# Performance work log

Hardware: AMD Instinct MI355X
Metric: run time of the kernel (lower is better)

## Reference

```python
import jax, jax.numpy as jnp
import numpy as np

D_MODEL = 1024
NUM_HEADS = 16
NUM_GROUPS = 4
HEAD_DIM = D_MODEL // NUM_HEADS
ROPE_BASE = 10000.0


def _rope_tables(seq_len, head_dim, dtype=jnp.float32):
    inv_freq = 1.0 / (ROPE_BASE ** (jnp.arange(0, head_dim, 2, dtype=jnp.float32) / head_dim))
    freqs = jnp.arange(seq_len, dtype=jnp.float32)[:, None] * inv_freq[None, :]  # [S, hd/2]
    emb = jnp.concatenate([freqs, freqs], axis=-1)  # [S, hd]
    return jnp.cos(emb).astype(dtype), jnp.sin(emb).astype(dtype)


def _rotate_half(t):
    half = t.shape[-1] // 2
    return jnp.concatenate([-t[..., half:], t[..., :half]], axis=-1)


def _apply_rope(t, cos, sin):
    # t: [B,S,H,hd]; cos/sin: [S,hd] broadcast over batch and heads
    c = cos[None, :, None, :]
    s = sin[None, :, None, :]
    return t * c + _rotate_half(t) * s


def setup_inputs() -> dict:
    key = jax.random.key(0)
    ks = jax.random.split(key, 5)
    B, S, D = 2, 2048, D_MODEL
    scale = 1.0 / np.sqrt(D)
    return {
        "x": jax.random.normal(ks[0], (B, S, D), dtype=jnp.float32),
        "Wq": jax.random.normal(ks[1], (D, D), dtype=jnp.float32) * scale,
        "Wk": jax.random.normal(ks[2], (D, D), dtype=jnp.float32) * scale,
        "Wv": jax.random.normal(ks[3], (D, D), dtype=jnp.float32) * scale,
        "Wo": jax.random.normal(ks[4], (D, D), dtype=jnp.float32) * scale,
    }


def reference(x, Wq, Wk, Wv, Wo):
    B, S, D = x.shape
    H, G, hd = NUM_HEADS, NUM_GROUPS, HEAD_DIM
    hpg = H // G  # heads per group

    q = (x @ Wq.T).reshape(B, S, H, hd)
    k = (x @ Wk.T).reshape(B, S, H, hd)
    v = (x @ Wv.T).reshape(B, S, H, hd)

    cos, sin = _rope_tables(S, hd, x.dtype)
    q = _apply_rope(q, cos, sin)
    k = _apply_rope(k, cos, sin)

    # query head reordering: [B,S,G,hpg,hd] -> transpose(2,3) -> [B,S,H,hd]
    q = q.reshape(B, S, G, hpg, hd).swapaxes(2, 3).reshape(B, S, H, hd)
    # GQA group-mean of K/V, then repeat back to H heads
    k = k.reshape(B, S, G, hpg, hd).mean(axis=3)  # [B,S,G,hd]
    v = v.reshape(B, S, G, hpg, hd).mean(axis=3)
    k = jnp.repeat(k, hpg, axis=2)  # [B,S,H,hd]
    v = jnp.repeat(v, hpg, axis=2)

    q = q.transpose(0, 2, 1, 3)  # [B,H,S,hd]
    k = k.transpose(0, 2, 1, 3)
    v = v.transpose(0, 2, 1, 3)

    scores = jnp.einsum('bhqd,bhkd->bhqk', q, k) / np.sqrt(hd)  # [B,H,S,S]
    probs = jax.nn.softmax(scores, axis=-1)
    attn = jnp.einsum('bhqk,bhkd->bhqd', probs, v)

    attn = attn.transpose(0, 2, 1, 3).reshape(B, S, D)
    return attn @ Wo.T
```

## Files before the change

kernel.cpp:

```cpp
#include <hip/hip_runtime.h>
#include <hip/hip_bf16.h>
#include <math.h>

#define B_ 2
#define S_ 2048
#define D_ 1024
#define H_ 16
#define G_ 4
#define HD_ 64

typedef float f32x4  __attribute__((ext_vector_type(4)));
typedef float f32x16 __attribute__((ext_vector_type(16)));
typedef short s16x8  __attribute__((ext_vector_type(8)));
typedef unsigned short u16x4 __attribute__((ext_vector_type(4)));
typedef unsigned int   u32x4 __attribute__((ext_vector_type(4)));

__device__ __forceinline__ unsigned short f2b(float f) {
    __hip_bfloat16 h = __float2bfloat16(f);
    return __builtin_bit_cast(unsigned short, h);
}
__device__ __forceinline__ unsigned cvtpk(float lo, float hi) {
    unsigned r;
    asm("v_cvt_pk_bf16_f32 %0, %1, %2" : "=v"(r) : "v"(lo), "v"(hi));
    return r;
}
__device__ __forceinline__ void plswap(unsigned &a, unsigned &b) {
    asm("v_permlane32_swap_b32 %0, %1" : "+v"(a), "+v"(b));
}

#define MFMA16(a, b, c) __builtin_amdgcn_mfma_f32_16x16x32_bf16(a, b, c, 0, 0, 0)
#define MFMA32(a, b, c) __builtin_amdgcn_mfma_f32_32x32x16_bf16(a, b, c, 0, 0, 0)

#define GLOAD16(gp, lp) __builtin_amdgcn_global_load_lds(                      \
    (const __attribute__((address_space(1))) void*)(gp),                      \
    (__attribute__((address_space(3))) void*)(lp), 16, 0, 0)

__global__ __launch_bounds__(256)
void prep_all(const float* __restrict__ x,  const float* __restrict__ Wq,
              const float* __restrict__ Wk, const float* __restrict__ Wv,
              const float* __restrict__ Wo,
              unsigned short* __restrict__ xb, unsigned short* __restrict__ wb,
              unsigned short* __restrict__ wob,
              float* __restrict__ cost, float* __restrict__ sint)
{
    const int NQ_WB = (1536*1024)/4;
    const int NQ_WO = (1024*1024)/4;
    const int NQ_X  = (B_*S_*D_)/4;
    int q = blockIdx.x*256 + threadIdx.x;
    if (q < NQ_WB) {
        const int idx = q*4, row = idx >> 10, c = idx & 1023;
        u16x4 o;
        if (row < 1024) {
            f32x4 v = *(const f32x4*)&Wq[(size_t)row*1024 + c];
            #pragma unroll
            for (int j = 0; j < 4; ++j) o[j] = f2b(v[j]);
        } else {
            const int rd = row - 1024, kv = rd >> 8, gd = rd & 255;
            const int g = gd >> 6, d = gd & 63;
            const float* W = kv ? Wv : Wk;
            f32x4 sum = {0.f, 0.f, 0.f, 0.f};
            #pragma unroll
            for (int p = 0; p < 4; ++p)
                sum += *(const f32x4*)&W[(size_t)((g*4 + p)*64 + d)*1024 + c];
            #pragma unroll
            for (int j = 0; j < 4; ++j) o[j] = f2b(sum[j]*0.25f);
        }
        *(u16x4*)&wb[idx] = o;
        return;
    }
    q -= NQ_WB;
    if (q < NQ_WO) {
        const int idx = q*4;
        f32x4 v = *(const f32x4*)&Wo[idx];
        u16x4 o;
        #pragma unroll
        for (int j = 0; j < 4; ++j) o[j] = f2b(v[j]);
        *(u16x4*)&wob[idx] = o;
        return;
    }
    q -= NQ_WO;
    if (q < NQ_X) {
        const int idx = q*4;
        f32x4 v = *(const f32x4*)&x[idx];
        u16x4 o;
        #pragma unroll
        for (int j = 0; j < 4; ++j) o[j] = f2b(v[j]);
        *(u16x4*)&xb[idx] = o;
        return;
    }
    q -= NQ_X;
    if (q < (S_*32)/4) {
        const int idx = q*4, s = idx >> 5, f0 = idx & 31;
        #pragma unroll
        for (int j = 0; j < 4; ++j) {
            const float f = (float)(f0 + j);
            const float fr = (float)s * powf(10000.0f, -f*(1.0f/32.0f));
            cost[idx + j] = cosf(fr);
            sint[idx + j] = sinf(fr);
        }
    }
}

template<int MODE>
__global__ __launch_bounds__(256)
void gemm_mfma(const unsigned short* __restrict__ Am,
               const unsigned short* __restrict__ Bm,
               unsigned short* __restrict__ qr,
               unsigned short* __restrict__ kr,
               unsigned short* __restrict__ vt,
               float* __restrict__ outf,
               const float* __restrict__ cost,
               const float* __restrict__ sint,
               int nbx)
{
    __shared__ unsigned short As[2][128*64];
    __shared__ unsigned short Bs[2][128*64];

    const int nwg = gridDim.x;
    const int cpx = nwg >> 3;
    const int bid = blockIdx.x;
    const int swz = (bid & 7)*cpx + (bid >> 3);
    const int bx = swz % nbx, by = swz / nbx;

    const int t  = threadIdx.x;
    const int w  = t >> 6, l = t & 63;
    const int lg = l >> 4, lr = l & 15;
    const int wr = w >> 1, wc = w & 1;

    const unsigned short* gA = Am + (size_t)by*128*D_;
    const unsigned short* gB = Bm + (size_t)bx*128*D_;

    const int srow = l >> 3;
    const int schk = (l & 7) ^ srow;

#define STAGE(buf, k0)                                                         \
    _Pragma("unroll")                                                          \
    for (int i_ = 0; i_ < 4; ++i_) {                                           \
        const int row_ = 32*w + 8*i_ + srow;                                   \
        GLOAD16(gA + (size_t)row_*D_ + (k0) + 8*schk, &As[buf][(32*w + 8*i_)*64]); \
        GLOAD16(gB + (size_t)row_*D_ + (k0) + 8*schk, &Bs[buf][(32*w + 8*i_)*64]); \
    }

    f32x4 acc[4][4] = {};

    STAGE(0, 0);
    #pragma unroll 1
    for (int kt = 0; kt < 16; ++kt) {
        const int cur = kt & 1;
        if (kt < 15) {
            STAGE(cur ^ 1, 64*(kt + 1));
            asm volatile("s_waitcnt vmcnt(8)" ::: "memory");
        } else {
            asm volatile("s_waitcnt vmcnt(0)" ::: "memory");
        }
        __builtin_amdgcn_s_barrier();

        #pragma unroll
        for (int kk = 0; kk < 2; ++kk) {
            s16x8 af[4], bfr[4];
            #pragma unroll
            for (int m = 0; m < 4; ++m) {
                const int row = 64*wr + 16*m + lr;
                af[m] = *(const s16x8*)&As[cur][row*64 + 8*((lg + 4*kk) ^ (row & 7))];
            }
            #pragma unroll
            for (int n = 0; n < 4; ++n) {
                const int col = 64*wc + 16*n + lr;
                bfr[n] = *(const s16x8*)&Bs[cur][col*64 + 8*((lg + 4*kk) ^ (col & 7))];
            }
            #pragma unroll
            for (int m = 0; m < 4; ++m)
                #pragma unroll
                for (int n = 0; n < 4; ++n)
                    acc[m][n] = MFMA16(af[m], bfr[n], acc[m][n]);
        }
        asm volatile("s_waitcnt lgkmcnt(0)" ::: "memory");
        __builtin_amdgcn_s_barrier();
    }
#undef STAGE

    if (MODE == 1) {
        #pragma unroll
        for (int m = 0; m < 4; ++m)
            #pragma unroll
            for (int r = 0; r < 4; ++r) {
                const int row = by*128 + 64*wr + 16*m + 4*lg + r;
                #pragma unroll
                for (int n = 0; n < 4; ++n)
                    outf[(size_t)row*D_ + bx*128 + 64*wc + 16*n + lr] = acc[m][n][r];
            }
        return;
    }

    if (bx < 10) {
        const float CQ = 0.18033688011112044f;
        #pragma unroll
        for (int m = 0; m < 4; ++m) {
            #pragma unroll
            for (int r = 0; r < 4; ++r) {
                const int row = by*128 + 64*wr + 16*m + 4*lg + r;
                const int b = row >> 11, s = row & (S_ - 1);
                const float c_lo = cost[s*32 + lr],      s_lo = sint[s*32 + lr];
                const float c_hi = cost[s*32 + 16 + lr], s_hi = sint[s*32 + 16 + lr];
                unsigned short vals[4];
                #pragma unroll
                for (int n = 0; n < 4; ++n) {
                    const float cc = (n & 1) ? c_hi : c_lo;
                    const float sn = (n & 1) ? s_hi : s_lo;
                    const float self = acc[m][n][r], part = acc[m][n ^ 2][r];
                    float rv = (n < 2) ? fmaf(self, cc, -part*sn)
                                       : fmaf(self, cc,  part*sn);
                    if (bx < 8) rv *= CQ;
                    vals[n] = f2b(rv);
                }
                size_t base;
                unsigned short* dst;
                if (bx < 8) {
                    const int hh = 2*bx + wc;
                    const int hp = (hh & 3)*4 + (hh >> 2);
                    base = (((size_t)b*H_ + hp)*S_ + s)*HD_;
                    dst = qr;
                } else {
                    const int g = (bx - 8)*2 + wc;
                    base = (((size_t)b*G_ + g)*S_ + s)*HD_;
                    dst = kr;
                }
                #pragma unroll
                for (int n = 0; n < 4; ++n) dst[base + 16*n + lr] = vals[n];
            }
        }
    } else {
        const int g = (bx - 10)*2 + wc;
        #pragma unroll
        for (int m = 0; m < 4; ++m) {
            const int row0 = by*128 + 64*wr + 16*m + 4*lg;
            const int b = row0 >> 11, s0 = row0 & (S_ - 1);
            #pragma unroll
            for (int n = 0; n < 4; ++n) {
                const int dd = 16*n + lr;
                u16x4 v;
                #pragma unroll
                for (int r = 0; r < 4; ++r) v[r] = f2b(acc[m][n][r]);
                *(u16x4*)&vt[(((size_t)b*G_ + g)*HD_ + dd)*S_ + s0] = v;
            }
        }
    }
}

__device__ __forceinline__ void stage128(const unsigned short* Kp, const unsigned short* Vp,
                                         unsigned short* ks, unsigned short* vs,
                                         int kt, int w, int l)
{
    const int srow = l >> 3;
    const int schk = (l & 7) ^ srow;
    const int vrow = l >> 4;
    #pragma unroll
    for (int i = 0; i < 4; ++i) {
        const int krow = 32*w + 8*i + srow;
        GLOAD16(Kp + ((size_t)(kt*128 + krow))*HD_ + 8*schk, ks + (32*w + 8*i)*64);
        const int d    = 16*w + 4*i + vrow;
        const int vchk = (l & 15) ^ (d & 7);
        GLOAD16(Vp + (size_t)d*S_ + kt*128 + 8*vchk, vs + (16*w + 4*i)*128);
    }
}

__global__ __launch_bounds__(256)
void flash_attn_mfma(const unsigned short* __restrict__ qr,
                     const unsigned short* __restrict__ kr,
                     const unsigned short* __restrict__ vt,
                     unsigned short* __restrict__ attnb)
{
    __shared__ unsigned short Ks[2][128*64];
    __shared__ unsigned short Vs[2][64*128];

    const int nqt = S_/128;
    const int bid = blockIdx.x;
    const int cpx = gridDim.x >> 3;
    const int swz = (bid & 7)*cpx + (bid >> 3);
    const int qt = swz % nqt;
    const int h  = (swz/nqt) % H_;
    const int b  = swz/(nqt*H_);
    const int g  = h >> 2;
    const int t  = threadIdx.x;
    const int w  = t >> 6;
    const int l  = t & 63;
    const int hi = l >> 5;
    const int li = l & 31;

    const unsigned short* Qp = qr + (((size_t)b*H_ + h)*S_ + (size_t)qt*128 + w*32)*HD_;
    const unsigned short* Kp = kr + ((size_t)b*G_ + g)*(size_t)S_*HD_;
    const unsigned short* Vp = vt + ((size_t)b*G_ + g)*(size_t)HD_*S_;

    s16x8 qf[4];
    #pragma unroll
    for (int kk = 0; kk < 4; ++kk)
        qf[kk] = *(const s16x8*)(Qp + (size_t)li*HD_ + 16*kk + 8*hi);

    s16x8 ones;
    #pragma unroll
    for (int e = 0; e < 8; ++e) ones[e] = (short)0x3F80;

    f32x16 o[2], o_l;
    #pragma unroll
    for (int e = 0; e < 16; ++e) { o[0][e] = 0.f; o[1][e] = 0.f; o_l[e] = 0.f; }

    const int NT = S_/128;
    stage128(Kp, Vp, Ks[0], Vs[0], 0, w, l);

    #pragma unroll 1
    for (int kt = 0; kt < NT; ++kt) {
        const int cur = kt & 1;
        if (kt + 1 < NT) {
            stage128(Kp, Vp, Ks[cur^1], Vs[cur^1], kt + 1, w, l);
            asm volatile("s_waitcnt vmcnt(8)" ::: "memory");
        } else {
            asm volatile("s_waitcnt vmcnt(0)" ::: "memory");
        }
        __builtin_amdgcn_s_barrier();

        f32x16 sc[4];
        #pragma unroll
        for (int q4 = 0; q4 < 4; ++q4)
            #pragma unroll
            for (int e = 0; e < 16; ++e) sc[q4][e] = 0.f;

        __builtin_amdgcn_s_setprio(1);
        #pragma unroll
        for (int kk = 0; kk < 4; ++kk) {
            const int chk = 8*((hi + 2*kk) ^ (li & 7));
            #pragma unroll
            for (int q4 = 0; q4 < 4; ++q4) {
                s16x8 kf = *(const s16x8*)&Ks[cur][(32*q4 + li)*64 + chk];
                sc[q4] = MFMA32(kf, qf[kk], sc[q4]);
            }
        }
        __builtin_amdgcn_s_setprio(0);

        #pragma unroll
        for (int q4 = 0; q4 < 4; ++q4)
            #pragma unroll
            for (int e = 0; e < 16; ++e)
                sc[q4][e] = __builtin_amdgcn_exp2f(sc[q4][e]);

        __builtin_amdgcn_s_setprio(1);
        #pragma unroll
        for (int q4 = 0; q4 < 4; ++q4) {
            #pragma unroll
            for (int s2 = 0; s2 < 2; ++s2) {
                unsigned a0 = cvtpk(sc[q4][8*s2+0], sc[q4][8*s2+1]);
                unsigned a1 = cvtpk(sc[q4][8*s2+2], sc[q4][8*s2+3]);
                unsigned a2 = cvtpk(sc[q4][8*s2+4], sc[q4][8*s2+5]);
                unsigned a3 = cvtpk(sc[q4][8*s2+6], sc[q4][8*s2+7]);
                plswap(a0, a2); plswap(a1, a3);
                u32x4 aw = {a0, a1, a2, a3};
                s16x8 paf = __builtin_bit_cast(s16x8, aw);
                const int ks = 2*q4 + s2;
                #pragma unroll
                for (int dt = 0; dt < 2; ++dt) {
                    const int d = li + 32*dt;
                    s16x8 vf = *(const s16x8*)&Vs[cur][d*128 + 8*((hi + 2*ks) ^ (li & 7))];
                    o[dt] = MFMA32(paf, vf, o[dt]);
                }
                o_l = MFMA32(paf, ones, o_l);
            }
        }
        __builtin_amdgcn_s_setprio(0);

        asm volatile("s_waitcnt lgkmcnt(0)" ::: "memory");
        __builtin_amdgcn_s_barrier();
    }

    #pragma unroll
    for (int r = 0; r < 16; ++r) {
        const int qq = (r & 3) + 8*(r >> 2) + 4*hi;
        const int s  = qt*128 + w*32 + qq;
        const float inv = 1.0f / o_l[r];
        #pragma unroll
        for (int dt = 0; dt < 2; ++dt)
            attnb[((size_t)b*S_ + s)*D_ + h*HD_ + li + 32*dt] = f2b(o[dt][r]*inv);
    }
}

extern "C" void kernel_launch(void* const* d_in, const int* in_sizes, int n_in,
                              void* d_out, int out_size, void* d_ws, size_t ws_size,
                              hipStream_t stream)
{
    const float* x  = (const float*)d_in[0];
    const float* Wq = (const float*)d_in[1];
    const float* Wk = (const float*)d_in[2];
    const float* Wv = (const float*)d_in[3];
    const float* Wo = (const float*)d_in[4];
    float* out = (float*)d_out;

    char* p = (char*)d_ws;
    unsigned short* xb    = (unsigned short*)p; p += (size_t)B_*S_*D_*2;
    unsigned short* wb    = (unsigned short*)p; p += (size_t)1536*1024*2;
    unsigned short* wob   = (unsigned short*)p; p += (size_t)1024*1024*2;
    unsigned short* qr    = (unsigned short*)p; p += (size_t)B_*H_*S_*HD_*2;
    unsigned short* kr    = (unsigned short*)p; p += (size_t)B_*G_*S_*HD_*2;
    unsigned short* vt    = (unsigned short*)p; p += (size_t)B_*G_*HD_*S_*2;
    unsigned short* attnb = (unsigned short*)p; p += (size_t)B_*S_*D_*2;
    float* cost = (float*)p; p += (size_t)S_*32*4;
    float* sint = (float*)p;

    prep_all<<<6720, 256, 0, stream>>>(x, Wq, Wk, Wv, Wo, xb, wb, wob, cost, sint);
    gemm_mfma<0><<<32*12, 256, 0, stream>>>(xb, wb, qr, kr, vt, nullptr, cost, sint, 12);
    flash_attn_mfma<<<B_*H_*(S_/128), 256, 0, stream>>>(qr, kr, vt, attnb);
    gemm_mfma<1><<<32*8, 256, 0, stream>>>(attnb, wob, nullptr, nullptr, nullptr, out, cost, sint, 8);
}
```

Measured before the change: 100.5 us.

## Split attention over key halves with a combine kernel and smaller key tiles

Each attention block now processes half of the key sequence with 64-key tiles, doubling the grid, and writes unnormalized partial outputs and row sums. A new combine kernel adds the two halves and normalizes them into the attention buffer. Workspace is rearranged so the partials reuse the region of the consumed bf16 input and weights. This aims at better CU occupancy and latency hiding, at the cost of an extra launch, extra memory traffic and bf16 rounding of the partials.

```diff
diff --git a/kernel.cpp b/kernel.cpp
--- a/kernel.cpp
+++ b/kernel.cpp
@@ -18,6 +18,9 @@
 __device__ __forceinline__ unsigned short f2b(float f) {
     __hip_bfloat16 h = __float2bfloat16(f);
     return __builtin_bit_cast(unsigned short, h);
+}
+__device__ __forceinline__ float b2f(unsigned short u) {
+    return __builtin_bit_cast(float, (unsigned)u << 16);
 }
 __device__ __forceinline__ unsigned cvtpk(float lo, float hi) {
     unsigned r;
@@ -247,49 +250,47 @@
     }
 }
 
-__device__ __forceinline__ void stage128(const unsigned short* Kp, const unsigned short* Vp,
-                                         unsigned short* ks, unsigned short* vs,
-                                         int kt, int w, int l)
+__device__ __forceinline__ void stage64(const unsigned short* Kp, const unsigned short* Vp,
+                                        unsigned short* ks, unsigned short* vs,
+                                        int key0, int w, int l)
 {
     const int srow = l >> 3;
     const int schk = (l & 7) ^ srow;
-    const int vrow = l >> 4;
-    #pragma unroll
-    for (int i = 0; i < 4; ++i) {
-        const int krow = 32*w + 8*i + srow;
-        GLOAD16(Kp + ((size_t)(kt*128 + krow))*HD_ + 8*schk, ks + (32*w + 8*i)*64);
-        const int d    = 16*w + 4*i + vrow;
-        const int vchk = (l & 15) ^ (d & 7);
-        GLOAD16(Vp + (size_t)d*S_ + kt*128 + 8*vchk, vs + (16*w + 4*i)*128);
-    }
-}
-
-__global__ __launch_bounds__(256)
+    #pragma unroll
+    for (int i = 0; i < 2; ++i) {
+        const int row = 16*w + 8*i + srow;
+        GLOAD16(Kp + ((size_t)(key0 + row))*HD_ + 8*schk, ks + (16*w + 8*i)*64);
+        GLOAD16(Vp + (size_t)row*S_ + key0 + 8*schk,      vs + (16*w + 8*i)*64);
+    }
+}
+
+__global__ __launch_bounds__(256, 4)
 void flash_attn_mfma(const unsigned short* __restrict__ qr,
                      const unsigned short* __restrict__ kr,
                      const unsigned short* __restrict__ vt,
-                     unsigned short* __restrict__ attnb)
-{
-    __shared__ unsigned short Ks[2][128*64];
-    __shared__ unsigned short Vs[2][64*128];
-
-    const int nqt = S_/128;
-    const int bid = blockIdx.x;
-    const int cpx = gridDim.x >> 3;
-    const int swz = (bid & 7)*cpx + (bid >> 3);
-    const int qt = swz % nqt;
-    const int h  = (swz/nqt) % H_;
-    const int b  = swz/(nqt*H_);
-    const int g  = h >> 2;
-    const int t  = threadIdx.x;
-    const int w  = t >> 6;
-    const int l  = t & 63;
-    const int hi = l >> 5;
-    const int li = l & 31;
+                     unsigned short* __restrict__ po,
+                     float* __restrict__ pl)
+{
+    __shared__ unsigned short Ks[2][64*64];
+    __shared__ unsigned short Vs[2][64*64];
+
+    const int bid  = blockIdx.x;
+    const int cpx  = gridDim.x >> 3;
+    const int swz  = (bid & 7)*cpx + (bid >> 3);
+    const int qt   = swz & 15;
+    const int h    = (swz >> 4) & 15;
+    const int b    = (swz >> 8) & 1;
+    const int half = swz >> 9;
+    const int g    = h >> 2;
+    const int t    = threadIdx.x;
+    const int w    = t >> 6;
+    const int l    = t & 63;
+    const int hi   = l >> 5;
+    const int li   = l & 31;
 
     const unsigned short* Qp = qr + (((size_t)b*H_ + h)*S_ + (size_t)qt*128 + w*32)*HD_;
-    const unsigned short* Kp = kr + ((size_t)b*G_ + g)*(size_t)S_*HD_;
-    const unsigned short* Vp = vt + ((size_t)b*G_ + g)*(size_t)HD_*S_;
+    const unsigned short* Kp = kr + ((size_t)b*G_ + g)*(size_t)S_*HD_ + (size_t)half*1024*HD_;
+    const unsigned short* Vp = vt + ((size_t)b*G_ + g)*(size_t)HD_*S_ + half*1024;
 
     s16x8 qf[4];
     #pragma unroll
@@ -304,23 +305,23 @@
     #pragma unroll
     for (int e = 0; e < 16; ++e) { o[0][e] = 0.f; o[1][e] = 0.f; o_l[e] = 0.f; }
 
-    const int NT = S_/128;
-    stage128(Kp, Vp, Ks[0], Vs[0], 0, w, l);
+    const int NT = 1024/64;
+    stage64(Kp, Vp, Ks[0], Vs[0], 0, w, l);
 
     #pragma unroll 1
     for (int kt = 0; kt < NT; ++kt) {
         const int cur = kt & 1;
         if (kt + 1 < NT) {
-            stage128(Kp, Vp, Ks[cur^1], Vs[cur^1], kt + 1, w, l);
-            asm volatile("s_waitcnt vmcnt(8)" ::: "memory");
+            stage64(Kp, Vp, Ks[cur^1], Vs[cur^1], 64*(kt + 1), w, l);
+            asm volatile("s_waitcnt vmcnt(4)" ::: "memory");
         } else {
             asm volatile("s_waitcnt vmcnt(0)" ::: "memory");
         }
         __builtin_amdgcn_s_barrier();
 
-        f32x16 sc[4];
-        #pragma unroll
-        for (int q4 = 0; q4 < 4; ++q4)
+        f32x16 sc[2];
+        #pragma unroll
+        for (int q4 = 0; q4 < 2; ++q4)
             #pragma unroll
             for (int e = 0; e < 16; ++e) sc[q4][e] = 0.f;
 
@@ -329,7 +330,7 @@
         for (int kk = 0; kk < 4; ++kk) {
             const int chk = 8*((hi + 2*kk) ^ (li & 7));
             #pragma unroll
-            for (int q4 = 0; q4 < 4; ++q4) {
+            for (int q4 = 0; q4 < 2; ++q4) {
                 s16x8 kf = *(const s16x8*)&Ks[cur][(32*q4 + li)*64 + chk];
                 sc[q4] = MFMA32(kf, qf[kk], sc[q4]);
             }
@@ -337,14 +338,14 @@
         __builtin_amdgcn_s_setprio(0);
 
         #pragma unroll
-        for (int q4 = 0; q4 < 4; ++q4)
+        for (int q4 = 0; q4 < 2; ++q4)
             #pragma unroll
             for (int e = 0; e < 16; ++e)
                 sc[q4][e] = __builtin_amdgcn_exp2f(sc[q4][e]);
 
         __builtin_amdgcn_s_setprio(1);
         #pragma unroll
-        for (int q4 = 0; q4 < 4; ++q4) {
+        for (int q4 = 0; q4 < 2; ++q4) {
             #pragma unroll
             for (int s2 = 0; s2 < 2; ++s2) {
                 unsigned a0 = cvtpk(sc[q4][8*s2+0], sc[q4][8*s2+1]);
@@ -358,7 +359,7 @@
                 #pragma unroll
                 for (int dt = 0; dt < 2; ++dt) {
                     const int d = li + 32*dt;
-                    s16x8 vf = *(const s16x8*)&Vs[cur][d*128 + 8*((hi + 2*ks) ^ (li & 7))];
+                    s16x8 vf = *(const s16x8*)&Vs[cur][d*64 + 8*((hi + 2*ks) ^ (li & 7))];
                     o[dt] = MFMA32(paf, vf, o[dt]);
                 }
                 o_l = MFMA32(paf, ones, o_l);
@@ -370,15 +371,40 @@
         __builtin_amdgcn_s_barrier();
     }
 
+    const size_t pbase = (((size_t)half*B_ + b)*H_ + h)*S_;
     #pragma unroll
     for (int r = 0; r < 16; ++r) {
         const int qq = (r & 3) + 8*(r >> 2) + 4*hi;
         const int s  = qt*128 + w*32 + qq;
-        const float inv = 1.0f / o_l[r];
         #pragma unroll
         for (int dt = 0; dt < 2; ++dt)
-            attnb[((size_t)b*S_ + s)*D_ + h*HD_ + li + 32*dt] = f2b(o[dt][r]*inv);
-    }
+            po[(pbase + s)*HD_ + li + 32*dt] = f2b(o[dt][r]);
+        if (li == 0) pl[pbase + s] = o_l[r];
+    }
+}
+
+__global__ __launch_bounds__(256)
+void combine_kernel(const unsigned short* __restrict__ po,
+                    const float* __restrict__ pl,
+                    unsigned short* __restrict__ attnb)
+{
+    const int i  = blockIdx.x*256 + threadIdx.x;
+    const int d8 = i & 7;
+    const int s  = (i >> 3) & (S_ - 1);
+    const int h  = (i >> 14) & (H_ - 1);
+    const int b  = i >> 18;
+    const size_t r0 = (((size_t)b)*H_ + h)*S_ + s;
+    const size_t r1 = (((size_t)B_ + b)*H_ + h)*S_ + s;
+    const float inv = 1.0f / (pl[r0] + pl[r1]);
+    s16x8 p0 = *(const s16x8*)&po[r0*HD_ + d8*8];
+    s16x8 p1 = *(const s16x8*)&po[r1*HD_ + d8*8];
+    s16x8 ov;
+    #pragma unroll
+    for (int j = 0; j < 8; ++j) {
+        const float v = (b2f((unsigned short)p0[j]) + b2f((unsigned short)p1[j])) * inv;
+        ov[j] = (short)f2b(v);
+    }
+    *(s16x8*)&attnb[((size_t)b*S_ + s)*D_ + h*HD_ + d8*8] = ov;
 }
 
 extern "C" void kernel_launch(void* const* d_in, const int* in_sizes, int n_in,
@@ -393,18 +419,22 @@
     float* out = (float*)d_out;
 
     char* p = (char*)d_ws;
-    unsigned short* xb    = (unsigned short*)p; p += (size_t)B_*S_*D_*2;
-    unsigned short* wb    = (unsigned short*)p; p += (size_t)1536*1024*2;
-    unsigned short* wob   = (unsigned short*)p; p += (size_t)1024*1024*2;
     unsigned short* qr    = (unsigned short*)p; p += (size_t)B_*H_*S_*HD_*2;
     unsigned short* kr    = (unsigned short*)p; p += (size_t)B_*G_*S_*HD_*2;
     unsigned short* vt    = (unsigned short*)p; p += (size_t)B_*G_*HD_*S_*2;
+    unsigned short* wob   = (unsigned short*)p; p += (size_t)1024*1024*2;
     unsigned short* attnb = (unsigned short*)p; p += (size_t)B_*S_*D_*2;
-    float* cost = (float*)p; p += (size_t)S_*32*4;
-    float* sint = (float*)p;
+    float* pl   = (float*)p;  p += (size_t)2*B_*H_*S_*4;
+    float* cost = (float*)p;  p += (size_t)S_*32*4;
+    float* sint = (float*)p;  p += (size_t)S_*32*4;
+    char* regionX = p;
+    unsigned short* xb = (unsigned short*)regionX;
+    unsigned short* wb = (unsigned short*)(regionX + (size_t)B_*S_*D_*2);
+    unsigned short* po = (unsigned short*)regionX;
 
     prep_all<<<6720, 256, 0, stream>>>(x, Wq, Wk, Wv, Wo, xb, wb, wob, cost, sint);
     gemm_mfma<0><<<32*12, 256, 0, stream>>>(xb, wb, qr, kr, vt, nullptr, cost, sint, 12);
-    flash_attn_mfma<<<B_*H_*(S_/128), 256, 0, stream>>>(qr, kr, vt, attnb);
+    flash_attn_mfma<<<B_*H_*(S_/128)*2, 256, 0, stream>>>(qr, kr, vt, po, pl);
+    combine_kernel<<<(B_*H_*S_*HD_/8)/256, 256, 0, stream>>>(po, pl, attnb);
     gemm_mfma<1><<<32*8, 256, 0, stream>>>(attnb, wob, nullptr, nullptr, nullptr, out, cost, sint, 8);
 }
```

Result: slower. 105.6 us (+5.1%).
